# Optimization experiments

Hardware: AMD Instinct MI355X
Metric: run time of the kernel (lower is better)

Reference implementation:

```python
import jax, jax.numpy as jnp
import numpy as np

N_DIM = 1024
HEAD_NUM = 16
HEAD_DIM = N_DIM // HEAD_NUM


def setup_inputs() -> dict:
    key = jax.random.key(0)
    ks = jax.random.split(key, 6)
    s = 1.0 / np.sqrt(N_DIM)
    return {
        "x": jax.random.normal(ks[0], (2, 2048, N_DIM), dtype=jnp.float32),
        "wq": jax.random.uniform(ks[1], (N_DIM, N_DIM), jnp.float32, -s, s),
        "wk": jax.random.uniform(ks[2], (N_DIM, N_DIM), jnp.float32, -s, s),
        "wv": jax.random.uniform(ks[3], (N_DIM, N_DIM), jnp.float32, -s, s),
        "wo": jax.random.uniform(ks[4], (N_DIM, N_DIM), jnp.float32, -s, s),
        "bo": jax.random.uniform(ks[5], (N_DIM,), jnp.float32, -s, s),
    }


def reference(x, wq, wk, wv, wo, bo):
    B, S, D = x.shape
    # torch Linear: y = x @ W.T
    def proj(w):
        return (x @ w.T).reshape(B, S, HEAD_NUM, HEAD_DIM).transpose(0, 2, 1, 3)  # [B,H,S,Dh]
    q, k, v = proj(wq), proj(wk), proj(wv)
    scale = 1.0 / np.sqrt(HEAD_DIM).astype(np.float32)
    scores = jnp.einsum("bhqd,bhkd->bhqk", q, k) * scale  # [B,H,S,S]
    attn = jax.nn.softmax(scores, axis=-1)
    y = jnp.einsum("bhqk,bhkd->bhqd", attn, v)  # [B,H,S,Dh]
    y = y.transpose(0, 2, 1, 3).reshape(B, S, D)
    return y @ wo.T + bo
```

## Files before the change

### kernel.cpp

```cpp
#include <hip/hip_runtime.h>
#include <math.h>

#define B_DIM 2
#define S_DIM 2048
#define D_DIM 1024
#define H_NUM 16
#define DH    64
#define M_DIM (B_DIM * S_DIM)

typedef __attribute__((ext_vector_type(8))) short short8;
typedef __attribute__((ext_vector_type(4))) short short4v;
typedef __attribute__((ext_vector_type(4))) float float4v;
typedef __attribute__((ext_vector_type(4))) unsigned short ushort4v;
typedef unsigned short ushort;

static __device__ __forceinline__ ushort f2bf(float f) {
    unsigned u = __float_as_uint(f);
    u += 0x7fffu + ((u >> 16) & 1u);
    return (ushort)(u >> 16);
}

static __device__ __forceinline__ float fexp2(float x) {
#if __has_builtin(__builtin_amdgcn_exp2f)
    return __builtin_amdgcn_exp2f(x);
#else
    return exp2f(x);
#endif
}

static __device__ __forceinline__ unsigned pack_bf16(float lo, float hi) {
    return (unsigned)f2bf(lo) | ((unsigned)f2bf(hi) << 16);
}

static __device__ __forceinline__ void gload_lds16(const void* g, void* l) {
    __builtin_amdgcn_global_load_lds(
        (const __attribute__((address_space(1))) void*)g,
        (__attribute__((address_space(3))) void*)l, 16, 0, 0);
}

__global__ __launch_bounds__(256)
void cast_all(const float* __restrict__ x,  const float* __restrict__ wq,
              const float* __restrict__ wk, const float* __restrict__ wv,
              const float* __restrict__ wo, ushort* __restrict__ dst)
{
    const int i = blockIdx.x * 256 + threadIdx.x;
    const float4* s;
    int off;
    if      (i < 1048576) { s = (const float4*)x;  off = 0;       }
    else if (i < 1310720) { s = (const float4*)wq; off = 1048576; }
    else if (i < 1572864) { s = (const float4*)wk; off = 1310720; }
    else if (i < 1835008) { s = (const float4*)wv; off = 1572864; }
    else                  { s = (const float4*)wo; off = 1835008; }
    const float4 v = s[i - off];
    ushort4v o;
    o[0] = f2bf(v.x); o[1] = f2bf(v.y); o[2] = f2bf(v.z); o[3] = f2bf(v.w);
    ((ushort4v*)dst)[i] = o;
}

__global__ __launch_bounds__(256)
void gemm_bf16(const ushort* __restrict__ A, const ushort* __restrict__ B,
               ushort* __restrict__ Qh, ushort* __restrict__ Kh,
               ushort* __restrict__ Vt, float* __restrict__ Of,
               const float* __restrict__ bias, int mode)
{
    __shared__ ushort Asm[128 * 32];
    __shared__ ushort Bsm[128 * 32];

    const int K  = 1024;
    const int n0 = blockIdx.x * 128;
    const int m0 = blockIdx.y * 128;
    const int t    = threadIdx.x;
    const int w    = t >> 6;
    const int lane = t & 63;
    const int n    = lane & 15;
    const int quad = lane >> 4;
    const int wm = w >> 1, wn = w & 1;

    const int srow = w * 32 + (lane >> 2);
    const int skel = (lane & 3) * 8;

    float4v acc[4][4];
#pragma unroll
    for (int mt = 0; mt < 4; ++mt)
#pragma unroll
        for (int nt = 0; nt < 4; ++nt) acc[mt][nt] = (float4v){0.f, 0.f, 0.f, 0.f};

    for (int kt = 0; kt < K; kt += 32) {
#pragma unroll
        for (int i = 0; i < 2; ++i) {
            gload_lds16(&A[(size_t)(m0 + srow + i * 16) * K + kt + skel],
                        &Asm[(w * 2 + i) * 512]);
            gload_lds16(&B[(size_t)(n0 + srow + i * 16) * K + kt + skel],
                        &Bsm[(w * 2 + i) * 512]);
        }
        __syncthreads();

        short8 af[4], bfr[4];
#pragma unroll
        for (int mt = 0; mt < 4; ++mt)
            af[mt] = *(const short8*)&Asm[(wm * 64 + mt * 16 + n) * 32 + quad * 8];
#pragma unroll
        for (int nt = 0; nt < 4; ++nt)
            bfr[nt] = *(const short8*)&Bsm[(wn * 64 + nt * 16 + n) * 32 + quad * 8];

#pragma unroll
        for (int mt = 0; mt < 4; ++mt)
#pragma unroll
            for (int nt = 0; nt < 4; ++nt)
                acc[mt][nt] = __builtin_amdgcn_mfma_f32_16x16x32_bf16(
                    af[mt], bfr[nt], acc[mt][nt], 0, 0, 0);
        __syncthreads();
    }

    if (mode == 0) {
        const int wid = n0 >> 10;
        ushort* dstQK = (wid == 0) ? Qh : Kh;
        const float qs = (wid == 0) ? 0.1803368801f : 1.0f;
#pragma unroll
        for (int mt = 0; mt < 4; ++mt) {
            const int m = m0 + wm * 64 + mt * 16 + quad * 4;
            const int b = m >> 11, s = m & (S_DIM - 1);
#pragma unroll
            for (int nt = 0; nt < 4; ++nt) {
                const int ng = (n0 & 1023) + wn * 64 + nt * 16 + n;
                const int h = ng >> 6, d = ng & 63;
                const int bh = b * H_NUM + h;
                if (wid < 2) {
#pragma unroll
                    for (int r = 0; r < 4; ++r)
                        dstQK[(((size_t)bh * S_DIM + s + r) << 6) + d] =
                            f2bf(acc[mt][nt][r] * qs);
                } else {
                    ushort4v p;
#pragma unroll
                    for (int r = 0; r < 4; ++r) p[r] = f2bf(acc[mt][nt][r]);
                    *(ushort4v*)&Vt[(((size_t)bh * DH + d) << 11) + s] = p;
                }
            }
        }
    } else {
#pragma unroll
        for (int mt = 0; mt < 4; ++mt) {
            const int m = m0 + wm * 64 + mt * 16 + quad * 4;
#pragma unroll
            for (int nt = 0; nt < 4; ++nt) {
                const int ng = n0 + wn * 64 + nt * 16 + n;
                const float bv = bias[ng];
#pragma unroll
                for (int r = 0; r < 4; ++r)
                    Of[(size_t)(m + r) * D_DIM + ng] = acc[mt][nt][r] + bv;
            }
        }
    }
}

__global__ __launch_bounds__(256)
void attn_mfma(const ushort* __restrict__ Qh, const ushort* __restrict__ Kh,
               const ushort* __restrict__ Vt, ushort* __restrict__ Yh)
{
    __shared__ ushort Ksm[2][64 * 64];
    __shared__ ushort Vsm[2][64 * 64];

    const int w    = threadIdx.x >> 6;
    const int lane = threadIdx.x & 63;
    const int n    = lane & 15;
    const int quad = lane >> 4;

    const int wave_id = blockIdx.x * 4 + w;
    const int bh    = wave_id >> 6;
    const int qbase = (wave_id & 63) * 32;
    const int b     = bh >> 4;
    const int h     = bh & (H_NUM - 1);

    const ushort* Qb = Qh + (((size_t)bh * S_DIM) << 6);
    const ushort* Kb = Kh + (((size_t)bh * S_DIM) << 6);
    const ushort* Vb = Vt + (((size_t)bh * DH) << 11);

    const int l8 = lane >> 3;
    const int sg = (lane & 7) ^ l8;

    short8 qa[2][2];
#pragma unroll
    for (int mt = 0; mt < 2; ++mt)
#pragma unroll
        for (int kc = 0; kc < 2; ++kc)
            qa[mt][kc] = *(const short8*)&Qb[((size_t)(qbase + mt * 16 + n) << 6) + kc * 32 + quad * 8];

    float4v O[2][4];
    float   mrow[2], lrow[2];
#pragma unroll
    for (int mt = 0; mt < 2; ++mt) {
#pragma unroll
        for (int nt = 0; nt < 4; ++nt) O[mt][nt] = (float4v){0.f, 0.f, 0.f, 0.f};
        mrow[mt] = -1e30f; lrow[mt] = 0.f;
    }

    const int fswz[2] = { ((0 * 4 + quad) ^ (n & 7)) * 8,
                          ((1 * 4 + quad) ^ (n & 7)) * 8 };
    const int h4 = (quad & 1) * 4;
    const int q2 = quad >> 1;
    int vswz[2][2];
#pragma unroll
    for (int kc = 0; kc < 2; ++kc)
#pragma unroll
        for (int cc = 0; cc < 2; ++cc)
            vswz[kc][cc] = (((4 * kc + 2 * cc + q2) ^ (n & 7)) << 3) + h4;

#pragma unroll
    for (int i = 0; i < 2; ++i) {
        gload_lds16(&Kb[(size_t)(w * 16 + i * 8 + l8) * 64 + sg * 8],
                    &Ksm[0][(w * 16 + i * 8) * 64]);
        gload_lds16(&Vb[(size_t)(w * 16 + i * 8 + l8) * 2048 + sg * 8],
                    &Vsm[0][(w * 16 + i * 8) * 64]);
    }

    for (int kb = 0; kb < S_DIM / 64; ++kb) {
        __syncthreads();
        const int cur = kb & 1;
        if (kb + 1 < S_DIM / 64) {
            const int key1 = (kb + 1) * 64;
            const int nxt  = cur ^ 1;
#pragma unroll
            for (int i = 0; i < 2; ++i) {
                gload_lds16(&Kb[(size_t)(key1 + w * 16 + i * 8 + l8) * 64 + sg * 8],
                            &Ksm[nxt][(w * 16 + i * 8) * 64]);
                gload_lds16(&Vb[(size_t)(w * 16 + i * 8 + l8) * 2048 + key1 + sg * 8],
                            &Vsm[nxt][(w * 16 + i * 8) * 64]);
            }
        }

        short8 kf[4][2];
#pragma unroll
        for (int ct = 0; ct < 4; ++ct)
#pragma unroll
            for (int kc = 0; kc < 2; ++kc)
                kf[ct][kc] = *(const short8*)&Ksm[cur][(ct * 16 + n) * 64 + fswz[kc]];

        float4v s[2][4];
#pragma unroll
        for (int mt = 0; mt < 2; ++mt)
#pragma unroll
            for (int ct = 0; ct < 4; ++ct) {
                float4v a = (float4v){0.f, 0.f, 0.f, 0.f};
                a = __builtin_amdgcn_mfma_f32_16x16x32_bf16(kf[ct][0], qa[mt][0], a, 0, 0, 0);
                a = __builtin_amdgcn_mfma_f32_16x16x32_bf16(kf[ct][1], qa[mt][1], a, 0, 0, 0);
                s[mt][ct] = a;
            }

        short8 vf[4][2];
#pragma unroll
        for (int nt = 0; nt < 4; ++nt) {
            const int rb = (nt * 16 + n) * 64;
#pragma unroll
            for (int kc = 0; kc < 2; ++kc) {
                const short4v g0 = *(const short4v*)&Vsm[cur][rb + vswz[kc][0]];
                const short4v g1 = *(const short4v*)&Vsm[cur][rb + vswz[kc][1]];
                vf[nt][kc] = __builtin_shufflevector(g0, g1, 0, 1, 2, 3, 4, 5, 6, 7);
            }
        }

#pragma unroll
        for (int mt = 0; mt < 2; ++mt) {
            float lm = s[mt][0][0];
#pragma unroll
            for (int ct = 0; ct < 4; ++ct)
#pragma unroll
                for (int r = 0; r < 4; ++r)
                    lm = fmaxf(lm, s[mt][ct][r]);
            lm = fmaxf(lm, __shfl_xor(lm, 16, 64));
            lm = fmaxf(lm, __shfl_xor(lm, 32, 64));

            const bool ev = lm > mrow[mt] + 8.0f;
            if (__any(ev)) {
                const float mnew  = ev ? lm : mrow[mt];
                const float alpha = fexp2(mrow[mt] - mnew);
                mrow[mt] = mnew;
                lrow[mt] *= alpha;
                const int ai = __float_as_int(alpha);
                float av[4];
#pragma unroll
                for (int r = 0; r < 4; ++r)
                    av[r] = __int_as_float(
                        __builtin_amdgcn_ds_bpermute(4 * (quad * 4 + r), ai));
#pragma unroll
                for (int nt = 0; nt < 4; ++nt)
#pragma unroll
                    for (int r = 0; r < 4; ++r) O[mt][nt][r] *= av[r];
            }

            float pv[4][4];
            float lsum = 0.f;
#pragma unroll
            for (int ct = 0; ct < 4; ++ct)
#pragma unroll
                for (int r = 0; r < 4; ++r) {
                    const float p = fexp2(s[mt][ct][r] - mrow[mt]);
                    pv[ct][r] = p;
                    lsum += p;
                }
            lrow[mt] += lsum;

            union { unsigned u[4]; short8 s8; } pk[2];
#pragma unroll
            for (int kc = 0; kc < 2; ++kc) {
                pk[kc].u[0] = pack_bf16(pv[2 * kc][0],     pv[2 * kc][1]);
                pk[kc].u[1] = pack_bf16(pv[2 * kc][2],     pv[2 * kc][3]);
                pk[kc].u[2] = pack_bf16(pv[2 * kc + 1][0], pv[2 * kc + 1][1]);
                pk[kc].u[3] = pack_bf16(pv[2 * kc + 1][2], pv[2 * kc + 1][3]);
            }

#pragma unroll
            for (int nt = 0; nt < 4; ++nt) {
                O[mt][nt] = __builtin_amdgcn_mfma_f32_16x16x32_bf16(pk[0].s8, vf[nt][0], O[mt][nt], 0, 0, 0);
                O[mt][nt] = __builtin_amdgcn_mfma_f32_16x16x32_bf16(pk[1].s8, vf[nt][1], O[mt][nt], 0, 0, 0);
            }
        }
    }

#pragma unroll
    for (int mt = 0; mt < 2; ++mt) {
        float ls = lrow[mt];
        ls += __shfl_xor(ls, 16, 64);
        ls += __shfl_xor(ls, 32, 64);
        const float linv = 1.f / ls;
        const int  li = __float_as_int(linv);
        float lv[4];
#pragma unroll
        for (int r = 0; r < 4; ++r)
            lv[r] = __int_as_float(
                __builtin_amdgcn_ds_bpermute(4 * (quad * 4 + r), li));
#pragma unroll
        for (int nt = 0; nt < 4; ++nt)
#pragma unroll
            for (int r = 0; r < 4; ++r) {
                const int q = qbase + mt * 16 + quad * 4 + r;
                Yh[((size_t)(b * S_DIM + q) << 10) + h * DH + nt * 16 + n] =
                    f2bf(O[mt][nt][r] * lv[r]);
            }
    }
}

extern "C" void kernel_launch(void* const* d_in, const int* in_sizes, int n_in,
                              void* d_out, int out_size, void* d_ws, size_t ws_size,
                              hipStream_t stream)
{
    const float* x  = (const float*)d_in[0];
    const float* wq = (const float*)d_in[1];
    const float* wk = (const float*)d_in[2];
    const float* wv = (const float*)d_in[3];
    const float* wo = (const float*)d_in[4];
    const float* bo = (const float*)d_in[5];
    float* out = (float*)d_out;

    const size_t MD = (size_t)M_DIM * D_DIM;
    const size_t WD = (size_t)D_DIM * D_DIM;
    ushort* xh  = (ushort*)d_ws;
    ushort* Wh  = xh + MD;
    ushort* Woh = Wh + 3 * WD;
    ushort* Qh  = Woh + WD;
    ushort* Kh  = Qh + MD;
    ushort* Vt  = Kh + MD;
    ushort* Yh  = Vt + MD;
    if (ws_size < 48u * 1024u * 1024u) return;

    dim3 blk(256);
    cast_all<<<dim3(8192), blk, 0, stream>>>(x, wq, wk, wv, wo, xh);

    gemm_bf16<<<dim3(24, 32), blk, 0, stream>>>(xh, Wh, Qh, Kh, Vt, nullptr, nullptr, 0);
    attn_mfma<<<dim3(512), blk, 0, stream>>>(Qh, Kh, Vt, Yh);
    gemm_bf16<<<dim3(8, 32), blk, 0, stream>>>(Yh, Woh, nullptr, nullptr, nullptr, out, bo, 1);
}
```

Measured before the change: 224.6 us.

## Halve per-wave query rows in attention and use hardware bf16 pack convert

Each attention wave now handles 16 query rows instead of 32, and the grid doubles to 1024 blocks. This gives more waves and lower register pressure, at the cost of loading each K/V tile into LDS twice as often per query. The software round-to-nearest bf16 packing of softmax probabilities is replaced with the v_cvt_pk_bf16_f32 instruction to cut ALU work in the inner loop.

Measured after the change: 243.1 us. 8.2% more time.

```diff
diff --git a/kernel.cpp b/kernel.cpp
--- a/kernel.cpp
+++ b/kernel.cpp
@@ -28,8 +28,10 @@
 #endif
 }
 
-static __device__ __forceinline__ unsigned pack_bf16(float lo, float hi) {
-    return (unsigned)f2bf(lo) | ((unsigned)f2bf(hi) << 16);
+static __device__ __forceinline__ unsigned cvtpk_bf16(float lo, float hi) {
+    unsigned r;
+    asm("v_cvt_pk_bf16_f32 %0, %1, %2" : "=v"(r) : "v"(lo), "v"(hi));
+    return r;
 }
 
 static __device__ __forceinline__ void gload_lds16(const void* g, void* l) {
@@ -167,8 +169,8 @@
     const int quad = lane >> 4;
 
     const int wave_id = blockIdx.x * 4 + w;
-    const int bh    = wave_id >> 6;
-    const int qbase = (wave_id & 63) * 32;
+    const int bh    = wave_id >> 7;
+    const int qbase = (wave_id & 127) * 16;
     const int b     = bh >> 4;
     const int h     = bh & (H_NUM - 1);
 
@@ -179,21 +181,16 @@
     const int l8 = lane >> 3;
     const int sg = (lane & 7) ^ l8;
 
-    short8 qa[2][2];
-#pragma unroll
-    for (int mt = 0; mt < 2; ++mt)
-#pragma unroll
-        for (int kc = 0; kc < 2; ++kc)
-            qa[mt][kc] = *(const short8*)&Qb[((size_t)(qbase + mt * 16 + n) << 6) + kc * 32 + quad * 8];
-
-    float4v O[2][4];
-    float   mrow[2], lrow[2];
-#pragma unroll
-    for (int mt = 0; mt < 2; ++mt) {
-#pragma unroll
-        for (int nt = 0; nt < 4; ++nt) O[mt][nt] = (float4v){0.f, 0.f, 0.f, 0.f};
-        mrow[mt] = -1e30f; lrow[mt] = 0.f;
-    }
+    short8 qa[2];
+#pragma unroll
+    for (int kc = 0; kc < 2; ++kc)
+        qa[kc] = *(const short8*)&Qb[((size_t)(qbase + n) << 6) + kc * 32 + quad * 8];
+
+    float4v O[4];
+    float   mrow, lrow;
+#pragma unroll
+    for (int nt = 0; nt < 4; ++nt) O[nt] = (float4v){0.f, 0.f, 0.f, 0.f};
+    mrow = -1e30f; lrow = 0.f;
 
     const int fswz[2] = { ((0 * 4 + quad) ^ (n & 7)) * 8,
                           ((1 * 4 + quad) ^ (n & 7)) * 8 };
@@ -236,16 +233,14 @@
             for (int kc = 0; kc < 2; ++kc)
                 kf[ct][kc] = *(const short8*)&Ksm[cur][(ct * 16 + n) * 64 + fswz[kc]];
 
-        float4v s[2][4];
-#pragma unroll
-        for (int mt = 0; mt < 2; ++mt)
-#pragma unroll
-            for (int ct = 0; ct < 4; ++ct) {
-                float4v a = (float4v){0.f, 0.f, 0.f, 0.f};
-                a = __builtin_amdgcn_mfma_f32_16x16x32_bf16(kf[ct][0], qa[mt][0], a, 0, 0, 0);
-                a = __builtin_amdgcn_mfma_f32_16x16x32_bf16(kf[ct][1], qa[mt][1], a, 0, 0, 0);
-                s[mt][ct] = a;
-            }
+        float4v s[4];
+#pragma unroll
+        for (int ct = 0; ct < 4; ++ct) {
+            float4v a = (float4v){0.f, 0.f, 0.f, 0.f};
+            a = __builtin_amdgcn_mfma_f32_16x16x32_bf16(kf[ct][0], qa[0], a, 0, 0, 0);
+            a = __builtin_amdgcn_mfma_f32_16x16x32_bf16(kf[ct][1], qa[1], a, 0, 0, 0);
+            s[ct] = a;
+        }
 
         short8 vf[4][2];
 #pragma unroll
@@ -259,85 +254,79 @@
             }
         }
 
-#pragma unroll
-        for (int mt = 0; mt < 2; ++mt) {
-            float lm = s[mt][0][0];
-#pragma unroll
-            for (int ct = 0; ct < 4; ++ct)
-#pragma unroll
-                for (int r = 0; r < 4; ++r)
-                    lm = fmaxf(lm, s[mt][ct][r]);
-            lm = fmaxf(lm, __shfl_xor(lm, 16, 64));
-            lm = fmaxf(lm, __shfl_xor(lm, 32, 64));
-
-            const bool ev = lm > mrow[mt] + 8.0f;
-            if (__any(ev)) {
-                const float mnew  = ev ? lm : mrow[mt];
-                const float alpha = fexp2(mrow[mt] - mnew);
-                mrow[mt] = mnew;
-                lrow[mt] *= alpha;
-                const int ai = __float_as_int(alpha);
-                float av[4];
-#pragma unroll
-                for (int r = 0; r < 4; ++r)
-                    av[r] = __int_as_float(
-                        __builtin_amdgcn_ds_bpermute(4 * (quad * 4 + r), ai));
-#pragma unroll
-                for (int nt = 0; nt < 4; ++nt)
-#pragma unroll
-                    for (int r = 0; r < 4; ++r) O[mt][nt][r] *= av[r];
-            }
-
-            float pv[4][4];
-            float lsum = 0.f;
-#pragma unroll
-            for (int ct = 0; ct < 4; ++ct)
-#pragma unroll
-                for (int r = 0; r < 4; ++r) {
-                    const float p = fexp2(s[mt][ct][r] - mrow[mt]);
-                    pv[ct][r] = p;
-                    lsum += p;
-                }
-            lrow[mt] += lsum;
-
-            union { unsigned u[4]; short8 s8; } pk[2];
-#pragma unroll
-            for (int kc = 0; kc < 2; ++kc) {
-                pk[kc].u[0] = pack_bf16(pv[2 * kc][0],     pv[2 * kc][1]);
-                pk[kc].u[1] = pack_bf16(pv[2 * kc][2],     pv[2 * kc][3]);
-                pk[kc].u[2] = pack_bf16(pv[2 * kc + 1][0], pv[2 * kc + 1][1]);
-                pk[kc].u[3] = pack_bf16(pv[2 * kc + 1][2], pv[2 * kc + 1][3]);
-            }
-
-#pragma unroll
-            for (int nt = 0; nt < 4; ++nt) {
-                O[mt][nt] = __builtin_amdgcn_mfma_f32_16x16x32_bf16(pk[0].s8, vf[nt][0], O[mt][nt], 0, 0, 0);
-                O[mt][nt] = __builtin_amdgcn_mfma_f32_16x16x32_bf16(pk[1].s8, vf[nt][1], O[mt][nt], 0, 0, 0);
-            }
+        float lm = s[0][0];
+#pragma unroll
+        for (int ct = 0; ct < 4; ++ct)
+#pragma unroll
+            for (int r = 0; r < 4; ++r)
+                lm = fmaxf(lm, s[ct][r]);
+        lm = fmaxf(lm, __shfl_xor(lm, 16, 64));
+        lm = fmaxf(lm, __shfl_xor(lm, 32, 64));
+
+        const bool ev = lm > mrow + 8.0f;
+        if (__any(ev)) {
+            const float mnew  = ev ? lm : mrow;
+            const float alpha = fexp2(mrow - mnew);
+            mrow = mnew;
+            lrow *= alpha;
+            const int ai = __float_as_int(alpha);
+            float av[4];
+#pragma unroll
+            for (int r = 0; r < 4; ++r)
+                av[r] = __int_as_float(
+                    __builtin_amdgcn_ds_bpermute(4 * (quad * 4 + r), ai));
+#pragma unroll
+            for (int nt = 0; nt < 4; ++nt)
+#pragma unroll
+                for (int r = 0; r < 4; ++r) O[nt][r] *= av[r];
+        }
+
+        float pv[4][4];
+        float lsum = 0.f;
+#pragma unroll
+        for (int ct = 0; ct < 4; ++ct)
+#pragma unroll
+            for (int r = 0; r < 4; ++r) {
+                const float p = fexp2(s[ct][r] - mrow);
+                pv[ct][r] = p;
+                lsum += p;
+            }
+        lrow += lsum;
+
+        union { unsigned u[4]; short8 s8; } pk[2];
+#pragma unroll
+        for (int kc = 0; kc < 2; ++kc) {
+            pk[kc].u[0] = cvtpk_bf16(pv[2 * kc][0],     pv[2 * kc][1]);
+            pk[kc].u[1] = cvtpk_bf16(pv[2 * kc][2],     pv[2 * kc][3]);
+            pk[kc].u[2] = cvtpk_bf16(pv[2 * kc + 1][0], pv[2 * kc + 1][1]);
+            pk[kc].u[3] = cvtpk_bf16(pv[2 * kc + 1][2], pv[2 * kc + 1][3]);
+        }
+
+#pragma unroll
+        for (int nt = 0; nt < 4; ++nt) {
+            O[nt] = __builtin_amdgcn_mfma_f32_16x16x32_bf16(pk[0].s8, vf[nt][0], O[nt], 0, 0, 0);
+            O[nt] = __builtin_amdgcn_mfma_f32_16x16x32_bf16(pk[1].s8, vf[nt][1], O[nt], 0, 0, 0);
         }
     }
 
-#pragma unroll
-    for (int mt = 0; mt < 2; ++mt) {
-        float ls = lrow[mt];
-        ls += __shfl_xor(ls, 16, 64);
-        ls += __shfl_xor(ls, 32, 64);
-        const float linv = 1.f / ls;
-        const int  li = __float_as_int(linv);
-        float lv[4];
-#pragma unroll
-        for (int r = 0; r < 4; ++r)
-            lv[r] = __int_as_float(
-                __builtin_amdgcn_ds_bpermute(4 * (quad * 4 + r), li));
-#pragma unroll
-        for (int nt = 0; nt < 4; ++nt)
-#pragma unroll
-            for (int r = 0; r < 4; ++r) {
-                const int q = qbase + mt * 16 + quad * 4 + r;
-                Yh[((size_t)(b * S_DIM + q) << 10) + h * DH + nt * 16 + n] =
-                    f2bf(O[mt][nt][r] * lv[r]);
-            }
-    }
+    float ls = lrow;
+    ls += __shfl_xor(ls, 16, 64);
+    ls += __shfl_xor(ls, 32, 64);
+    const float linv = 1.f / ls;
+    const int  li = __float_as_int(linv);
+    float lv[4];
+#pragma unroll
+    for (int r = 0; r < 4; ++r)
+        lv[r] = __int_as_float(
+            __builtin_amdgcn_ds_bpermute(4 * (quad * 4 + r), li));
+#pragma unroll
+    for (int nt = 0; nt < 4; ++nt)
+#pragma unroll
+        for (int r = 0; r < 4; ++r) {
+            const int q = qbase + quad * 4 + r;
+            Yh[((size_t)(b * S_DIM + q) << 10) + h * DH + nt * 16 + n] =
+                f2bf(O[nt][r] * lv[r]);
+        }
 }
 
 extern "C" void kernel_launch(void* const* d_in, const int* in_sizes, int n_in,
@@ -367,6 +356,6 @@
     cast_all<<<dim3(8192), blk, 0, stream>>>(x, wq, wk, wv, wo, xh);
 
     gemm_bf16<<<dim3(24, 32), blk, 0, stream>>>(xh, Wh, Qh, Kh, Vt, nullptr, nullptr, 0);
-    attn_mfma<<<dim3(512), blk, 0, stream>>>(Qh, Kh, Vt, Yh);
+    attn_mfma<<<dim3(1024), blk, 0, stream>>>(Qh, Kh, Vt, Yh);
     gemm_bf16<<<dim3(8, 32), blk, 0, stream>>>(Yh, Woh, nullptr, nullptr, nullptr, out, bo, 1);
 }
```
